# Kernel tuning notes

Measured on AMD Instinct MI355X. Metric: run time of the kernel, lower is better.

The kernel has to match this reference:

```python
import jax, jax.numpy as jnp
import numpy as np

K = 32  # neighbors per sampled point
EPS = 1e-5

def _layernorm(h, g, b):
    mu = jnp.mean(h, axis=-1, keepdims=True)
    var = jnp.mean((h - mu) ** 2, axis=-1, keepdims=True)
    return (h - mu) * jax.lax.rsqrt(var + EPS) * g + b


def setup_inputs() -> dict:
    key = jax.random.key(0)
    ks = jax.random.split(key, 20)
    N, M, D_IN, D_T = 32768, 4096, 64, 128
    s = lambda k, *sh: jax.random.normal(k, sh, dtype=jnp.float32) * 0.05
    inp = {
        "x": jax.random.normal(ks[0], (N, D_IN), dtype=jnp.float32),
        "pos": jax.random.normal(ks[1], (N, 3), dtype=jnp.float32),
        "idx": jax.random.randint(ks[2], (M,), 0, N, dtype=jnp.int32),
        "batch": jnp.zeros((N,), dtype=jnp.int32),
        # PointNetConv MLP [67 -> 128 -> 256] (ReLU after first layer only)
        "W1": s(ks[3], D_IN + 3, 128), "b1": jnp.zeros((128,), jnp.float32),
        "W2": s(ks[4], 128, 256),     "b2": jnp.zeros((256,), jnp.float32),
        # feature_reduction Linear(256, 128)
        "Wr": s(ks[5], 256, D_T), "br": jnp.zeros((D_T,), jnp.float32),
        # MultiheadAttention(128, 4)
        "in_proj_w": s(ks[6], D_T, 3 * D_T), "in_proj_b": jnp.zeros((3 * D_T,), jnp.float32),
        "out_proj_w": s(ks[7], D_T, D_T),    "out_proj_b": jnp.zeros((D_T,), jnp.float32),
        # transformer MLP [128 -> 256 -> 128]
        "Wm1": s(ks[8], D_T, 2 * D_T), "bm1": jnp.zeros((2 * D_T,), jnp.float32),
        "Wm2": s(ks[9], 2 * D_T, D_T), "bm2": jnp.zeros((D_T,), jnp.float32),
        # layer norms
        "g1": jnp.ones((D_T,), jnp.float32), "beta1": jnp.zeros((D_T,), jnp.float32),
        "g2": jnp.ones((D_T,), jnp.float32), "beta2": jnp.zeros((D_T,), jnp.float32),
    }
    return inp


def _forward(x, pos, idx, batch, W1, b1, W2, b2, Wr, br,
             in_proj_w, in_proj_b, out_proj_w, out_proj_b,
             Wm1, bm1, Wm2, bm2, g1, beta1, g2, beta2):
    q_pos = pos[idx]                                    # [M,3]
    # KNN: k nearest source points for each sampled (dst) point
    d2 = (jnp.sum(q_pos ** 2, -1, keepdims=True)
          - 2.0 * (q_pos @ pos.T)
          + jnp.sum(pos ** 2, -1)[None, :])             # [M,N]
    _, col = jax.lax.top_k(-d2, K)                      # [M,K] source indices
    # PointNetConv message: nn([x_j, pos_j - pos_i]), max-aggregate per dst
    x_j = x[col]                                        # [M,K,64]
    rel = pos[col] - q_pos[:, None, :]                  # [M,K,3]
    feat = jnp.concatenate([x_j, rel], axis=-1)         # [M,K,67]
    h = jax.nn.relu(feat @ W1 + b1) @ W2 + b2           # [M,K,256]
    agg = jnp.max(h, axis=1)                            # [M,256]
    xt = agg @ Wr + br                                  # [M,128]
    # TransformerBlock: x.view(M,1,128) -> MHA over seq len M, batch 1
    M, D = xt.shape
    H = 4
    Dh = D // H
    qkv = xt @ in_proj_w + in_proj_b                    # [M,3D]
    qh, kh, vh = [t.reshape(M, H, Dh) for t in jnp.split(qkv, 3, axis=-1)]
    scores = jnp.einsum('qhd,khd->hqk', qh, kh) / np.sqrt(Dh)
    attn = jax.nn.softmax(scores, axis=-1)
    att = jnp.einsum('hqk,khd->qhd', attn, vh).reshape(M, D)
    att = att @ out_proj_w + out_proj_b
    xt = _layernorm(xt + att, g1, beta1)
    mlp = jax.nn.relu(xt @ Wm1 + bm1) @ Wm2 + bm2
    xt = _layernorm(xt + mlp, g2, beta2)
    return xt, q_pos, batch[idx]


def reference(x, pos, idx, batch, W1, b1, W2, b2, Wr, br,
              in_proj_w, in_proj_b, out_proj_w, out_proj_b,
              Wm1, bm1, Wm2, bm2, g1, beta1, g2, beta2):
    return _forward(x, pos, idx, batch, W1, b1, W2, b2, Wr, br,
                    in_proj_w, in_proj_b, out_proj_w, out_proj_b,
                    Wm1, bm1, Wm2, bm2, g1, beta1, g2, beta2)
```

## Files before the change

### kernel.cpp

```cpp
#include <hip/hip_runtime.h>
#include <hip/hip_bf16.h>

#define DEV static __device__ __forceinline__

typedef __attribute__((ext_vector_type(8))) short          s16x8;
typedef __attribute__((ext_vector_type(8))) unsigned short u16x8;
typedef __attribute__((ext_vector_type(4))) float          f32x4;
typedef __attribute__((ext_vector_type(4))) unsigned int   u32x4;

#define MFMA16(A,B,C) __builtin_amdgcn_mfma_f32_16x16x32_bf16((A),(B),(C),0,0,0)

DEV unsigned short f2bf(float f) {
  unsigned int u = __builtin_bit_cast(unsigned int, f);
  u += 0x7fffu + ((u >> 16) & 1u);
  return (unsigned short)(u >> 16);
}
DEV float bf2f(unsigned short u) {
  unsigned int x = ((unsigned int)u) << 16;
  return __builtin_bit_cast(float, x);
}

#define QSCL 0.25503562201f

#define GRID_LO  (-5.0f)
#define GRID_IH  (3.2f)

DEV int cellc(float v) {
  int c = (int)floorf((v - GRID_LO) * GRID_IH);
  return min(31, max(0, c));
}

constexpr size_t OFF_POS4  = 0;
constexpr size_t OFF_COL   = 524288;
constexpr size_t OFF_W1T   = 1048576;
constexpr size_t OFF_W2T   = OFF_W1T  + 24576;
constexpr size_t OFF_WRT   = OFF_W2T  + 65536;
constexpr size_t OFF_WQKVT = OFF_WRT  + 65536;
constexpr size_t OFF_WOUTT = OFF_WQKVT+ 98304;
constexpr size_t OFF_WM1T  = OFF_WOUTT+ 32768;
constexpr size_t OFF_WM2T  = OFF_WM1T + 65536;
constexpr size_t OFF_H     = OFF_WM2T + 65536;
constexpr size_t OFF_SPOS    = OFF_H;
constexpr size_t OFF_CELLCNT = OFF_H + 524288;
constexpr size_t OFF_CELLDSC = OFF_H + 655360;
constexpr size_t OFF_FILL    = OFF_H + 917504;
constexpr size_t OFF_PO      = OFF_H;
constexpr size_t OFF_PL      = OFF_H + 16777216;
constexpr size_t OFF_AGG   = OFF_H    + 33554432;
constexpr size_t OFF_XT0   = OFF_AGG  + 4194304;
constexpr size_t OFF_QKV   = OFF_XT0  + 2097152;
constexpr size_t OFF_ATT   = OFF_QKV  + 6291456;
constexpr size_t OFF_PRE   = OFF_ATT  + 2097152;
constexpr size_t OFF_XT1   = OFF_PRE  + 2097152;
constexpr size_t OFF_MLP1  = OFF_XT1  + 2097152;
constexpr size_t OFF_SBIAS = OFF_MLP1 + 4194304;

__global__ __launch_bounds__(256) void zero_k(int* __restrict__ p) {
  p[blockIdx.x * 256 + threadIdx.x] = 0;
}

__global__ __launch_bounds__(256) void prep_k(
    const float* __restrict__ pos, const float* __restrict__ W1,
    const float* __restrict__ W2, const float* __restrict__ Wr,
    const float* __restrict__ ipw, const float* __restrict__ ipb,
    const float* __restrict__ opw,
    const float* __restrict__ Wm1, const float* __restrict__ Wm2,
    float4* __restrict__ pos4, unsigned short* __restrict__ w1t,
    unsigned short* __restrict__ w2t, unsigned short* __restrict__ wrt,
    unsigned short* __restrict__ wqkvt, unsigned short* __restrict__ woutt,
    unsigned short* __restrict__ wm1t, unsigned short* __restrict__ wm2t,
    int* __restrict__ cellcnt, float* __restrict__ sbias) {
  int T = blockIdx.x * 256 + threadIdx.x;
  if (T < 32768) {
    float px = pos[T*3], py = pos[T*3+1], pz = pos[T*3+2];
    pos4[T] = make_float4(px, py, pz, 0.f);
    int cid = (cellc(pz)*32 + cellc(py))*32 + cellc(px);
    atomicAdd(&cellcnt[cid], 1);
    return;
  }
  T -= 32768;
  if (T < 128*96)  { int n=T/96,  k=T%96;  w1t[T]  = f2bf(k < 67 ? W1[k*128+n] : 0.f); return; }
  T -= 128*96;
  if (T < 256*128) { int n=T/128, k=T%128; w2t[T]  = f2bf(W2[k*256+n]);  return; }
  T -= 256*128;
  if (T < 128*256) { int n=T/256, k=T%256; wrt[T]  = f2bf(Wr[k*128+n]);  return; }
  T -= 128*256;
  if (T < 384*128) { int n=T/128, k=T%128;
                     float v = ipw[k*384+n];
                     if (n < 128) v *= QSCL;
                     wqkvt[T]= f2bf(v); return; }
  T -= 384*128;
  if (T < 128*128) { int n=T/128, k=T%128; woutt[T]= f2bf(opw[k*128+n]); return; }
  T -= 128*128;
  if (T < 256*128) { int n=T/128, k=T%128; wm1t[T] = f2bf(Wm1[k*256+n]); return; }
  T -= 256*128;
  if (T < 128*256) { int n=T/256, k=T%256; wm2t[T] = f2bf(Wm2[k*128+n]); return; }
  T -= 128*256;
  if (T < 384) { sbias[T] = ipb[T] * (T < 128 ? QSCL : 1.f); return; }
}

__global__ __launch_bounds__(1024) void prefix_k(const int* __restrict__ cnt,
                                                 int2* __restrict__ desc,
                                                 int* __restrict__ fill) {
  __shared__ int wsum[16];
  const int tid = threadIdx.x, lane = tid & 63, w = tid >> 6;
  int loc[32]; int s = 0;
  #pragma unroll
  for (int i = 0; i < 32; ++i) { loc[i] = cnt[tid*32 + i]; s += loc[i]; }
  int sc = s;
  #pragma unroll
  for (int off = 1; off < 64; off <<= 1) {
    int v = __shfl_up(sc, off);
    if (lane >= off) sc += v;
  }
  if (lane == 63) wsum[w] = sc;
  __syncthreads();
  if (tid == 0) {
    int run = 0;
    #pragma unroll
    for (int i = 0; i < 16; ++i) { int v = wsum[i]; wsum[i] = run; run += v; }
  }
  __syncthreads();
  int base = wsum[w] + (sc - s);
  #pragma unroll
  for (int i = 0; i < 32; ++i) {
    int c = tid*32 + i;
    desc[c] = make_int2(base, loc[i]);
    fill[c] = base;
    base += loc[i];
  }
}

__global__ __launch_bounds__(256) void scatter_k(const float4* __restrict__ pos4,
                                                 int* __restrict__ fill,
                                                 float4* __restrict__ spos) {
  int T = blockIdx.x * 256 + threadIdx.x;
  float4 p = pos4[T];
  int cid = (cellc(p.z)*32 + cellc(p.y))*32 + cellc(p.x);
  int slot = atomicAdd(&fill[cid], 1);
  spos[slot] = make_float4(p.x, p.y, p.z, __int_as_float(T));
}

#define KNN_CAP  320
#define KNN_TRIG 192
#define KNN_KEEP 33
#define KNN_INF  3e37f

__global__ __launch_bounds__(256) void knn_k(
    const float4* __restrict__ spos, const int2* __restrict__ desc,
    const float4* __restrict__ pos4, const int* __restrict__ idx,
    int* __restrict__ col,
    float* __restrict__ outqpos, float* __restrict__ outbatch) {
  __shared__ float bufd[4][KNN_CAP];
  __shared__ int   bufi[4][KNN_CAP];
  __shared__ int   shist[4][64];
  __shared__ int2  segs[4][128];
  const int tid = threadIdx.x, lane = tid & 63, w = tid >> 6;
  const unsigned long long ltmask = (1ull << lane) - 1ull;

  const int q = blockIdx.x * 4 + w;
  const int iq = idx[q];
  const float4 qp = pos4[iq];
  const float qx = qp.x, qy = qp.y, qz = qp.z;
  const int cx0 = cellc(qx), cy0 = cellc(qy), cz0 = cellc(qz);

  float t = KNN_INF;
  int cnt = 0;

  auto compact = [&]() {
    int c_ = min(cnt, KNN_CAP);
    float vd[5]; int vi[5], bs[5]; bool okv[5];
    float dmax = 1e-30f;
    #pragma unroll
    for (int s = 0; s < 5; ++s) {
      int o2 = s*64 + lane;
      okv[s] = o2 < c_;
      vd[s] = okv[s] ? bufd[w][o2] : 0.f;
      vi[s] = okv[s] ? bufi[w][o2] : 0;
      dmax = fmaxf(dmax, vd[s]);
    }
    #pragma unroll
    for (int off = 1; off < 64; off <<= 1) dmax = fmaxf(dmax, __shfl_xor(dmax, off));
    float scale = 63.99f / dmax;
    shist[w][lane] = 0;
    #pragma unroll
    for (int s = 0; s < 5; ++s) {
      bs[s] = okv[s] ? min(63, (int)(vd[s] * scale)) : 64;
      if (okv[s]) atomicAdd(&shist[w][bs[s]], 1);
    }
    int h = shist[w][lane];
    #pragma unroll
    for (int off = 1; off < 64; off <<= 1) {
      int v = __shfl_up(h, off);
      if (lane >= off) h += v;
    }
    unsigned long long mk = __ballot(h >= KNN_KEEP);
    int E = mk ? (__ffsll((long long)mk) - 1) : 63;
    int base = 0;
    #pragma unroll
    for (int s = 0; s < 5; ++s) {
      bool keep = okv[s] && bs[s] <= E;
      unsigned long long km = __ballot(keep);
      int pp = base + (int)__popcll(km & ltmask);
      if (keep) { bufd[w][pp] = vd[s]; bufi[w][pp] = vi[s]; }
      base += (int)__popcll(km);
    }
    cnt = base;
    t = fminf(t, (float)(E + 1) / scale);
  };

  auto scan_rows = [&](int knew, int kold) {
    const int S = 2*knew + 1;
    const int NR = S*S;
    const float invS = 1.f / (float)S;
    for (int r0 = 0; r0 < NR; r0 += 64) {
      int r = r0 + lane;
      bool v = r < NR;
      int dz = (int)((float)r * invS);
      int rem = r - dz*S;
      if (rem < 0) { dz--; rem += S; } else if (rem >= S) { dz++; rem -= S; }
      int ccz = cz0 + dz - knew, ccy = cy0 + rem - knew;
      bool rowok = v && ccz >= 0 && ccz < 32 && ccy >= 0 && ccy < 32;
      bool inner = kold >= 0 && abs(dz - knew) <= kold && abs(rem - knew) <= kold;
      int cbase = (ccz*32 + ccy) * 32;
      int sL = 0, lL = 0, sR = 0, lR = 0;
      if (rowok) {
        int xa = max(cx0 - knew, 0);
        int xb = inner ? (cx0 - kold - 1) : min(cx0 + knew, 31);
        if (xa <= xb) {
          int2 d0 = desc[cbase + xa];
          int2 d1 = desc[cbase + xb];
          sL = d0.x; lL = d1.x + d1.y - d0.x;
        }
        if (inner) {
          int xa2 = cx0 + kold + 1, xb2 = min(cx0 + knew, 31);
          if (xa2 <= xb2 && xa2 >= 0) {
            int2 d0 = desc[cbase + xa2];
            int2 d1 = desc[cbase + xb2];
            sR = d0.x; lR = d1.x + d1.y - d0.x;
          }
        }
      }
      int cumL = lL;
      #pragma unroll
      for (int off = 1; off < 64; off <<= 1) {
        int vv = __shfl_up(cumL, off);
        if (lane >= off) cumL += vv;
      }
      int sumL = __shfl(cumL, 63);
      int cumR = lR;
      #pragma unroll
      for (int off = 1; off < 64; off <<= 1) {
        int vv = __shfl_up(cumR, off);
        if (lane >= off) cumR += vv;
      }
      int sumR = __shfl(cumR, 63);
      segs[w][lane]      = make_int2(sL, cumL - lL);
      segs[w][64 + lane] = make_int2(sR, sumL + cumR - lR);
      const int total = sumL + sumR;

      for (int b = 0; b < total; b += 320) {
        float d2v[5]; int piv[5]; bool hv[5];
        #pragma unroll
        for (int s5 = 0; s5 < 5; ++s5) {
          int p = b + s5*64 + lane;
          bool act = p < total;
          hv[s5] = false; d2v[s5] = 0.f; piv[s5] = 0;
          if (act) {
            int lo = 0;
            #pragma unroll
            for (int st = 64; st > 0; st >>= 1)
              if (segs[w][lo + st].y <= p) lo += st;
            int2 e = segs[w][lo];
            float4 pt = spos[e.x + (p - e.y)];
            float ddx = qx-pt.x, ddy = qy-pt.y, ddz = qz-pt.z;
            float d2 = ddx*ddx + ddy*ddy + ddz*ddz;
            d2v[s5] = d2; piv[s5] = __float_as_int(pt.w);
            hv[s5] = d2 < t;
          }
        }
        #pragma unroll
        for (int s5 = 0; s5 < 5; ++s5) {
          unsigned long long hm = __ballot(hv[s5]);
          if (hm) {
            int pp = cnt + (int)__popcll(hm & ltmask);
            if (hv[s5] && pp < KNN_CAP) { bufd[w][pp] = d2v[s5]; bufi[w][pp] = piv[s5]; }
            cnt += (int)__popcll(hm);
            if (cnt >= KNN_TRIG) compact();
          }
        }
      }
    }
  };

  auto bound32 = [&]() -> float {
    int c_ = min(cnt, KNN_CAP);
    float vv[5]; bool okv[5];
    float dmax = 1e-30f;
    #pragma unroll
    for (int s = 0; s < 5; ++s) {
      int o2 = s*64 + lane;
      okv[s] = o2 < c_;
      vv[s] = okv[s] ? bufd[w][o2] : 0.f;
      dmax = fmaxf(dmax, vv[s]);
    }
    #pragma unroll
    for (int off = 1; off < 64; off <<= 1) dmax = fmaxf(dmax, __shfl_xor(dmax, off));
    float scale = 63.99f / dmax;
    shist[w][lane] = 0;
    #pragma unroll
    for (int s = 0; s < 5; ++s)
      if (okv[s]) atomicAdd(&shist[w][min(63, (int)(vv[s] * scale))], 1);
    int h = shist[w][lane];
    #pragma unroll
    for (int off = 1; off < 64; off <<= 1) {
      int v = __shfl_up(h, off);
      if (lane >= off) h += v;
    }
    unsigned long long m = __ballot(h >= 32);
    int E = m ? (__ffsll((long long)m) - 1) : 63;
    return (float)(E + 1) / scale;
  };

  int kcur = 1;
  scan_rows(1, -1);
  for (int it = 0; it < 64; ++it) {
    if (cnt >= 32) {
      float t32u = bound32();
      t = fminf(t, t32u);
      int kneed = (int)(__builtin_sqrtf(t32u) * GRID_IH) + 1;
      if (kneed <= kcur || kcur >= 31) break;
      int knew = min(kneed, 31);
      scan_rows(knew, kcur);
      kcur = knew;
    } else {
      if (kcur >= 31) break;
      int knew = min(kcur + (cnt == 0 ? 2 : 1), 31);
      scan_rows(knew, kcur);
      kcur = knew;
    }
  }

  {
    int c_ = min(cnt, KNN_CAP);
    float vd[5]; int vi[5], bs[5]; bool okf[5];
    float dmax = 1e-30f;
    #pragma unroll
    for (int s = 0; s < 5; ++s) {
      int o2 = s*64 + lane;
      okf[s] = o2 < c_;
      vd[s] = okf[s] ? bufd[w][o2] : KNN_INF;
      vi[s] = okf[s] ? bufi[w][o2] : 0;
      dmax = fmaxf(dmax, okf[s] ? vd[s] : 0.f);
    }
    #pragma unroll
    for (int off = 1; off < 64; off <<= 1) dmax = fmaxf(dmax, __shfl_xor(dmax, off));
    float sc64 = 63.99f / dmax;
    shist[w][lane] = 0;
    #pragma unroll
    for (int s = 0; s < 5; ++s) {
      bs[s] = okf[s] ? min(63, (int)(vd[s] * sc64)) : 64;
      if (okf[s]) atomicAdd(&shist[w][bs[s]], 1);
    }
    int h = shist[w][lane];
    #pragma unroll
    for (int off = 1; off < 64; off <<= 1) {
      int v = __shfl_up(h, off);
      if (lane >= off) h += v;
    }
    unsigned long long m = __ballot(h >= 32);
    int E = m ? (__ffsll((long long)m) - 1) : 63;
    int c0 = (E > 0) ? __shfl(h, E - 1) : 0;
    int base = 0;
    #pragma unroll
    for (int s = 0; s < 5; ++s) {
      bool wr = okf[s] && (bs[s] < E);
      unsigned long long km = __ballot(wr);
      int pp = base + (int)__popcll(km & ltmask);
      if (wr) col[q*32 + pp] = vi[s];
      base += (int)__popcll(km);
    }
    #pragma unroll
    for (int s = 0; s < 5; ++s)
      if (!(okf[s] && bs[s] == E)) vd[s] = KNN_INF;
    int r = 32 - c0;
    #pragma unroll 1
    for (int kk = 0; kk < r; ++kk) {
      float bd = vd[0]; int bi = vi[0]; int bc = lane*8;
      #pragma unroll
      for (int s = 1; s < 5; ++s)
        if (vd[s] < bd) { bd = vd[s]; bi = vi[s]; bc = lane*8 + s; }
      #pragma unroll
      for (int off = 1; off < 64; off <<= 1) {
        float od = __shfl_xor(bd, off);
        int   oi = __shfl_xor(bi, off);
        int   oc = __shfl_xor(bc, off);
        if (od < bd || (od == bd && oc < bc)) { bd = od; bi = oi; bc = oc; }
      }
      if ((bc >> 3) == lane) {
        int sl = bc & 7;
        #pragma unroll
        for (int s = 0; s < 5; ++s) if (sl == s) vd[s] = KNN_INF;
      }
      if (lane == 0) col[q*32 + c0 + kk] = bi;
    }
  }
  if (lane == 0) {
    outqpos[q*3+0] = qx; outqpos[q*3+1] = qy; outqpos[q*3+2] = qz;
    outbatch[q] = 0.f;
  }
}

#define LA1(r,c) S[(r)*104 + (c)]
#define LB1(r,c) S[13312 + (r)*104 + (c)]
#define HB(r,c)  S[(r)*136 + (c)]
#define W2C(r,c) S[17408 + (r)*136 + (c)]

__global__ __launch_bounds__(256) void conv_k(
    const float* __restrict__ x, const float4* __restrict__ pos4,
    const int* __restrict__ idx, const int* __restrict__ col,
    const unsigned short* __restrict__ w1t, const float* __restrict__ b1,
    const unsigned short* __restrict__ w2t, const float* __restrict__ b2,
    float* __restrict__ agg) {
  __shared__ __align__(16) unsigned short S[26624];
  __shared__ int   sci[128];
  __shared__ float sqp[4][3];
  const int tid = threadIdx.x, lane = tid & 63, w = tid >> 6;
  const int wm = w >> 1, wn = w & 1;
  const int m0 = blockIdx.x * 4;

  if (tid < 128) sci[tid] = col[m0*32 + tid];
  if (tid >= 128 && tid < 132) {
    int m = m0 + tid - 128;
    float4 p = pos4[idx[m]];
    sqp[tid-128][0] = p.x; sqp[tid-128][1] = p.y; sqp[tid-128][2] = p.z;
  }
  #pragma unroll
  for (int rnd = 0; rnd < 6; ++rnd) {
    int e = (rnd*256 + tid) * 8;
    int n = e / 96, k = e % 96;
    *(u16x8*)&LB1(n, k) = *(const u16x8*)&w1t[e];
  }
  __syncthreads();

  {
    int r = tid >> 1, half = tid & 1;
    int ci = sci[r];
    const float* src = x + (size_t)ci*64 + half*32;
    #pragma unroll
    for (int c = 0; c < 4; ++c) {
      float4 va = ((const float4*)src)[c*2], vb = ((const float4*)src)[c*2+1];
      u16x8 v;
      v[0]=f2bf(va.x); v[1]=f2bf(va.y); v[2]=f2bf(va.z); v[3]=f2bf(va.w);
      v[4]=f2bf(vb.x); v[5]=f2bf(vb.y); v[6]=f2bf(vb.z); v[7]=f2bf(vb.w);
      *(u16x8*)&LA1(r, half*32 + c*8) = v;
    }
  }
  if (tid < 128) {
    int r = tid, g = r >> 5;
    float4 p = pos4[sci[r]];
    u16x8 z;
    #pragma unroll
    for (int e = 0; e < 8; ++e) z[e] = 0;
    u16x8 v0 = z;
    v0[0] = f2bf(p.x - sqp[g][0]); v0[1] = f2bf(p.y - sqp[g][1]); v0[2] = f2bf(p.z - sqp[g][2]);
    *(u16x8*)&LA1(r, 64) = v0;
    #pragma unroll
    for (int c = 1; c < 5; ++c) *(u16x8*)&LA1(r, 64 + c*8) = z;
  }
  __syncthreads();

  f32x4 acc[4][4];
  #pragma unroll
  for (int nf = 0; nf < 4; ++nf) {
    float bv = b1[wn*64 + nf*16 + (lane & 15)];
    #pragma unroll
    for (int mf = 0; mf < 4; ++mf) acc[mf][nf] = f32x4{bv, bv, bv, bv};
  }
  #pragma unroll
  for (int kc = 0; kc < 3; ++kc) {
    s16x8 af[4], bf_[4];
    #pragma unroll
    for (int mf = 0; mf < 4; ++mf)
      af[mf] = *(const s16x8*)&LA1(wm*64 + mf*16 + (lane&15), kc*32 + (lane>>4)*8);
    #pragma unroll
    for (int nf = 0; nf < 4; ++nf)
      bf_[nf] = *(const s16x8*)&LB1(wn*64 + nf*16 + (lane&15), kc*32 + (lane>>4)*8);
    #pragma unroll
    for (int mf = 0; mf < 4; ++mf)
      #pragma unroll
      for (int nf = 0; nf < 4; ++nf)
        acc[mf][nf] = MFMA16(af[mf], bf_[nf], acc[mf][nf]);
  }
  __syncthreads();

  #pragma unroll
  for (int mf = 0; mf < 4; ++mf)
    #pragma unroll
    for (int nf = 0; nf < 4; ++nf)
      #pragma unroll
      for (int j = 0; j < 4; ++j) {
        int rloc = wm*64 + mf*16 + ((lane>>4)<<2) + j;
        int cloc = wn*64 + nf*16 + (lane & 15);
        HB(rloc, cloc) = f2bf(fmaxf(acc[mf][nf][j], 0.f));
      }
  {
    int r2 = tid >> 2, kq = (tid & 3) * 32;
    const unsigned short* src = w2t + (size_t)r2*128 + kq;
    #pragma unroll
    for (int c = 0; c < 4; ++c)
      *(u16x8*)&W2C(r2, kq + c*8) = *(const u16x8*)&src[c*8];
  }
  __syncthreads();

  #pragma unroll 1
  for (int nc = 0; nc < 4; ++nc) {
    f32x4 acc2[2][4];
    #pragma unroll
    for (int nf = 0; nf < 4; ++nf) {
      float bv = b2[nc*64 + nf*16 + (lane & 15)];
      acc2[0][nf] = f32x4{bv, bv, bv, bv};
      acc2[1][nf] = f32x4{bv, bv, bv, bv};
    }
    #pragma unroll
    for (int ks = 0; ks < 4; ++ks) {
      s16x8 af[2], bf_[4];
      #pragma unroll
      for (int mf = 0; mf < 2; ++mf)
        af[mf] = *(const s16x8*)&HB(w*32 + mf*16 + (lane&15), ks*32 + (lane>>4)*8);
      #pragma unroll
      for (int nf = 0; nf < 4; ++nf)
        bf_[nf] = *(const s16x8*)&W2C(nf*16 + (lane&15), ks*32 + (lane>>4)*8);
      #pragma unroll
      for (int mf = 0; mf < 2; ++mf)
        #pragma unroll
        for (int nf = 0; nf < 4; ++nf)
          acc2[mf][nf] = MFMA16(af[mf], bf_[nf], acc2[mf][nf]);
    }
    #pragma unroll
    for (int nf = 0; nf < 4; ++nf) {
      float mx = acc2[0][nf][0];
      #pragma unroll
      for (int j = 1; j < 4; ++j) mx = fmaxf(mx, acc2[0][nf][j]);
      #pragma unroll
      for (int j = 0; j < 4; ++j) mx = fmaxf(mx, acc2[1][nf][j]);
      mx = fmaxf(mx, __shfl_xor(mx, 16));
      mx = fmaxf(mx, __shfl_xor(mx, 32));
      if (lane < 16) agg[(size_t)(m0 + w)*256 + nc*64 + nf*16 + lane] = mx;
    }
    if (nc < 3) {
      __syncthreads();
      int r2 = tid >> 2, kq = (tid & 3) * 32;
      const unsigned short* src = w2t + (size_t)((nc+1)*64 + r2)*128 + kq;
      #pragma unroll
      for (int c = 0; c < 4; ++c)
        *(u16x8*)&W2C(r2, kq + c*8) = *(const u16x8*)&src[c*8];
      __syncthreads();
    }
  }
}

template<int KFULL, int NFULL, bool RELU, bool HAS_RES, bool OBF16>
__global__ __launch_bounds__(256) void gemm_k(
    const float* __restrict__ A, const unsigned short* __restrict__ Bt,
    const float* __restrict__ bias, const float* __restrict__ res,
    float* __restrict__ out) {
  __shared__ unsigned short lA[64][72];
  __shared__ unsigned short lB[64][72];
  const int tid = threadIdx.x, lane = tid & 63, w = tid >> 6;
  const int m0 = blockIdx.x * 64, n0 = blockIdx.y * 64;

  f32x4 acc[4];
  #pragma unroll
  for (int nf = 0; nf < 4; ++nf) {
    float bv = bias[n0 + nf*16 + (lane & 15)];
    acc[nf] = f32x4{bv, bv, bv, bv};
  }

  for (int kb = 0; kb < KFULL; kb += 64) {
    __syncthreads();
    {
      int r = tid >> 2, kq = (tid & 3) * 16;
      const float* src = A + (size_t)(m0 + r)*KFULL + kb + kq;
      #pragma unroll
      for (int c = 0; c < 2; ++c) {
        float4 va = ((const float4*)src)[c*2], vb = ((const float4*)src)[c*2+1];
        u16x8 v;
        v[0]=f2bf(va.x); v[1]=f2bf(va.y); v[2]=f2bf(va.z); v[3]=f2bf(va.w);
        v[4]=f2bf(vb.x); v[5]=f2bf(vb.y); v[6]=f2bf(vb.z); v[7]=f2bf(vb.w);
        *(u16x8*)&lA[r][kq + c*8] = v;
      }
      const unsigned short* srcb = Bt + (size_t)(n0 + r)*KFULL + kb + kq;
      #pragma unroll
      for (int c = 0; c < 2; ++c)
        *(u16x8*)&lB[r][kq + c*8] = *(const u16x8*)&srcb[c*8];
    }
    __syncthreads();
    #pragma unroll
    for (int ks = 0; ks < 2; ++ks) {
      s16x8 af = *(const s16x8*)&lA[w*16 + (lane&15)][ks*32 + (lane>>4)*8];
      s16x8 bf_[4];
      #pragma unroll
      for (int nf = 0; nf < 4; ++nf)
        bf_[nf] = *(const s16x8*)&lB[nf*16 + (lane&15)][ks*32 + (lane>>4)*8];
      #pragma unroll
      for (int nf = 0; nf < 4; ++nf)
        acc[nf] = MFMA16(af, bf_[nf], acc[nf]);
    }
  }
  #pragma unroll
  for (int nf = 0; nf < 4; ++nf)
    #pragma unroll
    for (int j = 0; j < 4; ++j) {
      int row = m0 + w*16 + ((lane>>4)<<2) + j;
      int colg = n0 + nf*16 + (lane & 15);
      float v = acc[nf][j];
      if (HAS_RES) v += res[(size_t)row*NFULL + colg];
      if (RELU)    v = fmaxf(v, 0.f);
      if (OBF16) ((unsigned short*)out)[(size_t)row*NFULL + colg] = f2bf(v);
      else       out[(size_t)row*NFULL + colg] = v;
    }
}

template<int KFULL, bool COMBINE>
__global__ __launch_bounds__(256) void gemmln2_k(
    const float* __restrict__ A,
    const unsigned short* __restrict__ po, const float* __restrict__ pl,
    const unsigned short* __restrict__ Bt, const float* __restrict__ bias,
    const float* __restrict__ res,
    const float* __restrict__ gam, const float* __restrict__ bet,
    float* __restrict__ out) {
  constexpr int KP = KFULL + 8;
  __shared__ __align__(16) unsigned short lA[16 * KP];
  __shared__ float vout[16 * 132];
  const int tid = threadIdx.x, lane = tid & 63, w = tid >> 6;
  const int g = lane >> 4, ln_ = lane & 15;
  const int m0 = blockIdx.x * 16;

  {
    int r = tid >> 4, seg = tid & 15;
    int row = m0 + r;
    if (COMBINE) {
      int hh = seg >> 2;
      float lsum = 0.f;
      #pragma unroll
      for (int s = 0; s < 4; ++s) lsum += pl[((s*4 + hh) << 12) + row];
      float inv = 1.f / lsum;
      float a[8] = {0,0,0,0,0,0,0,0};
      #pragma unroll
      for (int s = 0; s < 4; ++s) {
        u16x8 v = *(const u16x8*)&po[((size_t)s*4096 + row)*128 + seg*8];
        #pragma unroll
        for (int e = 0; e < 8; ++e) a[e] += bf2f(v[e]);
      }
      u16x8 ov;
      #pragma unroll
      for (int e = 0; e < 8; ++e) ov[e] = f2bf(a[e] * inv);
      *(u16x8*)&lA[r*KP + seg*8] = ov;
    } else {
      const float* src = A + (size_t)row*KFULL + seg*(KFULL/16);
      #pragma unroll
      for (int c = 0; c < KFULL/128; ++c) {
        float4 va = ((const float4*)src)[c*2], vb = ((const float4*)src)[c*2+1];
        u16x8 v;
        v[0]=f2bf(va.x); v[1]=f2bf(va.y); v[2]=f2bf(va.z); v[3]=f2bf(va.w);
        v[4]=f2bf(vb.x); v[5]=f2bf(vb.y); v[6]=f2bf(vb.z); v[7]=f2bf(vb.w);
        *(u16x8*)&lA[r*KP + seg*(KFULL/16) + c*8] = v;
      }
    }
  }
  __syncthreads();

  const int n0 = w * 32;
  f32x4 acc[2];
  #pragma unroll
  for (int nf = 0; nf < 2; ++nf) {
    float bv = bias[n0 + nf*16 + ln_];
    acc[nf] = f32x4{bv, bv, bv, bv};
  }
  #pragma unroll
  for (int ks = 0; ks < KFULL/32; ++ks) {
    s16x8 af = *(const s16x8*)&lA[ln_*KP + ks*32 + g*8];
    #pragma unroll
    for (int nf = 0; nf < 2; ++nf) {
      s16x8 bf_ = *(const s16x8*)&Bt[(size_t)(n0 + nf*16 + ln_)*KFULL + ks*32 + g*8];
      acc[nf] = MFMA16(af, bf_, acc[nf]);
    }
  }
  #pragma unroll
  for (int nf = 0; nf < 2; ++nf)
    #pragma unroll
    for (int j = 0; j < 4; ++j)
      vout[(g*4 + j)*132 + n0 + nf*16 + ln_] = acc[nf][j];
  __syncthreads();

  {
    int r = tid >> 4, seg = tid & 15;
    int row = m0 + r;
    float v[8]; float sm = 0.f;
    #pragma unroll
    for (int nf = 0; nf < 8; ++nf) {
      int c = nf*16 + seg;
      float xx = vout[r*132 + c] + res[(size_t)row*128 + c];
      v[nf] = xx; sm += xx;
    }
    sm += __shfl_xor(sm, 1); sm += __shfl_xor(sm, 2);
    sm += __shfl_xor(sm, 4); sm += __shfl_xor(sm, 8);
    float mu = sm * 0.0078125f;
    float qv = 0.f;
    #pragma unroll
    for (int nf = 0; nf < 8; ++nf) { float d = v[nf] - mu; qv += d*d; }
    qv += __shfl_xor(qv, 1); qv += __shfl_xor(qv, 2);
    qv += __shfl_xor(qv, 4); qv += __shfl_xor(qv, 8);
    float rr = rsqrtf(qv * 0.0078125f + 1e-5f);
    #pragma unroll
    for (int nf = 0; nf < 8; ++nf) {
      int c = nf*16 + seg;
      out[(size_t)row*128 + c] = (v[nf] - mu) * rr * gam[c] + bet[c];
    }
  }
}

__global__ __launch_bounds__(256) void mlpln_k(
    const float* __restrict__ xt1,
    const unsigned short* __restrict__ wm1t, const float* __restrict__ bm1,
    const unsigned short* __restrict__ wm2t, const float* __restrict__ bm2,
    const float* __restrict__ gam, const float* __restrict__ bet,
    float* __restrict__ out) {
  __shared__ __align__(16) unsigned short lA[16 * 136];
  __shared__ __align__(16) unsigned short lH[16 * 264];
  __shared__ float vout[16 * 132];
  const int tid = threadIdx.x, lane = tid & 63, w = tid >> 6;
  const int g = lane >> 4, ln_ = lane & 15;
  const int m0 = blockIdx.x * 16;

  {
    int r = tid >> 4, seg = tid & 15;
    const float* src = xt1 + (size_t)(m0 + r)*128 + seg*8;
    float4 va = ((const float4*)src)[0], vb = ((const float4*)src)[1];
    u16x8 v;
    v[0]=f2bf(va.x); v[1]=f2bf(va.y); v[2]=f2bf(va.z); v[3]=f2bf(va.w);
    v[4]=f2bf(vb.x); v[5]=f2bf(vb.y); v[6]=f2bf(vb.z); v[7]=f2bf(vb.w);
    *(u16x8*)&lA[r*136 + seg*8] = v;
  }
  __syncthreads();

  {
    const int n0 = w * 64;
    f32x4 acc1[4];
    #pragma unroll
    for (int nf = 0; nf < 4; ++nf) {
      float bv = bm1[n0 + nf*16 + ln_];
      acc1[nf] = f32x4{bv, bv, bv, bv};
    }
    #pragma unroll
    for (int ks = 0; ks < 4; ++ks) {
      s16x8 af = *(const s16x8*)&lA[ln_*136 + ks*32 + g*8];
      #pragma unroll
      for (int nf = 0; nf < 4; ++nf) {
        s16x8 bf_ = *(const s16x8*)&wm1t[(size_t)(n0 + nf*16 + ln_)*128 + ks*32 + g*8];
        acc1[nf] = MFMA16(af, bf_, acc1[nf]);
      }
    }
    #pragma unroll
    for (int nf = 0; nf < 4; ++nf)
      #pragma unroll
      for (int j = 0; j < 4; ++j)
        lH[(g*4 + j)*264 + n0 + nf*16 + ln_] = f2bf(fmaxf(acc1[nf][j], 0.f));
  }
  __syncthreads();

  {
    const int n0 = w * 32;
    f32x4 acc2[2];
    #pragma unroll
    for (int nf = 0; nf < 2; ++nf) {
      float bv = bm2[n0 + nf*16 + ln_];
      acc2[nf] = f32x4{bv, bv, bv, bv};
    }
    #pragma unroll
    for (int ks = 0; ks < 8; ++ks) {
      s16x8 af = *(const s16x8*)&lH[ln_*264 + ks*32 + g*8];
      #pragma unroll
      for (int nf = 0; nf < 2; ++nf) {
        s16x8 bf_ = *(const s16x8*)&wm2t[(size_t)(n0 + nf*16 + ln_)*256 + ks*32 + g*8];
        acc2[nf] = MFMA16(af, bf_, acc2[nf]);
      }
    }
    #pragma unroll
    for (int nf = 0; nf < 2; ++nf)
      #pragma unroll
      for (int j = 0; j < 4; ++j)
        vout[(g*4 + j)*132 + n0 + nf*16 + ln_] = acc2[nf][j];
  }
  __syncthreads();

  {
    int r = tid >> 4, seg = tid & 15;
    int row = m0 + r;
    float v[8]; float sm = 0.f;
    #pragma unroll
    for (int nf = 0; nf < 8; ++nf) {
      int c = nf*16 + seg;
      float xx = vout[r*132 + c] + xt1[(size_t)row*128 + c];
      v[nf] = xx; sm += xx;
    }
    sm += __shfl_xor(sm, 1); sm += __shfl_xor(sm, 2);
    sm += __shfl_xor(sm, 4); sm += __shfl_xor(sm, 8);
    float mu = sm * 0.0078125f;
    float qv = 0.f;
    #pragma unroll
    for (int nf = 0; nf < 8; ++nf) { float d = v[nf] - mu; qv += d*d; }
    qv += __shfl_xor(qv, 1); qv += __shfl_xor(qv, 2);
    qv += __shfl_xor(qv, 4); qv += __shfl_xor(qv, 8);
    float rr = rsqrtf(qv * 0.0078125f + 1e-5f);
    #pragma unroll
    for (int nf = 0; nf < 8; ++nf) {
      int c = nf*16 + seg;
      out[(size_t)row*128 + c] = (v[nf] - mu) * rr * gam[c] + bet[c];
    }
  }
}

__global__ __launch_bounds__(256) void attn_k(
    const unsigned short* __restrict__ qkvb,
    unsigned short* __restrict__ po, float* __restrict__ pl) {
  __shared__ unsigned short lK[128][40];
  __shared__ unsigned short lV[32][136];
  const int tid = threadIdx.x, lane = tid & 63, w = tid >> 6;
  const int hh = blockIdx.y, sp = blockIdx.z;
  const int qr = blockIdx.x * 64 + w * 16;
  const int g = lane >> 4, q = lane & 15;

  s16x8 qf = *(const s16x8*)&qkvb[(size_t)(qr + q)*384 + hh*32 + g*8];

  f32x4 o[2];
  o[0] = f32x4{0.f,0.f,0.f,0.f}; o[1] = f32x4{0.f,0.f,0.f,0.f};
  float lrun = 0.f;

  const int srcA = q | ((2*(g & 1)) << 4);
  const int srcB = srcA + 16;
  const bool hi = (g >> 1) != 0;

  for (int kt = sp*8; kt < sp*8 + 8; ++kt) {
    const int k0 = kt * 128;
    __syncthreads();
    {
      int key = tid >> 1, d0 = (tid & 1) * 16;
      const unsigned short* src = qkvb + (size_t)(k0 + key)*384 + 128 + hh*32 + d0;
      *(u16x8*)&lK[key][d0]     = *(const u16x8*)&src[0];
      *(u16x8*)&lK[key][d0 + 8] = *(const u16x8*)&src[8];
    }
    {
      int kp = tid & 63, gg = tid >> 6;
      const unsigned short* s0 = qkvb + (size_t)(k0 + 2*kp)*384 + 256 + hh*32 + gg*8;
      u16x8 e0 = *(const u16x8*)s0;
      u16x8 e1 = *(const u16x8*)(s0 + 384);
      #pragma unroll
      for (int d = 0; d < 8; ++d) {
        unsigned int pkk = (unsigned int)e0[d] | ((unsigned int)e1[d] << 16);
        *(unsigned int*)&lV[gg*8 + d][2*kp] = pkk;
      }
    }
    __syncthreads();

    unsigned int pk[8][2];
    float ps = 0.f;
    #pragma unroll
    for (int nf = 0; nf < 8; ++nf) {
      s16x8 kf = *(const s16x8*)&lK[nf*16 + q][g*8];
      f32x4 c = MFMA16(kf, qf, (f32x4{0.f,0.f,0.f,0.f}));
      float p0 = exp2f(c[0]), p1 = exp2f(c[1]);
      float p2 = exp2f(c[2]), p3 = exp2f(c[3]);
      ps += (p0 + p1) + (p2 + p3);
      unsigned int u0 = __builtin_bit_cast(unsigned int, p0) + 0x8000u;
      unsigned int u1 = __builtin_bit_cast(unsigned int, p1) + 0x8000u;
      unsigned int u2 = __builtin_bit_cast(unsigned int, p2) + 0x8000u;
      unsigned int u3 = __builtin_bit_cast(unsigned int, p3) + 0x8000u;
      pk[nf][0] = (u0 >> 16) | (u1 & 0xffff0000u);
      pk[nf][1] = (u2 >> 16) | (u3 & 0xffff0000u);
    }
    ps += __shfl_xor(ps, 16);
    ps += __shfl_xor(ps, 32);
    lrun += ps;

    #pragma unroll
    for (int kc = 0; kc < 4; ++kc) {
      unsigned int a0 = (unsigned int)__shfl((int)pk[2*kc][0],   srcA);
      unsigned int b0 = (unsigned int)__shfl((int)pk[2*kc+1][0], srcA);
      unsigned int a1 = (unsigned int)__shfl((int)pk[2*kc][1],   srcA);
      unsigned int b1 = (unsigned int)__shfl((int)pk[2*kc+1][1], srcA);
      unsigned int a2 = (unsigned int)__shfl((int)pk[2*kc][0],   srcB);
      unsigned int b2 = (unsigned int)__shfl((int)pk[2*kc+1][0], srcB);
      unsigned int a3 = (unsigned int)__shfl((int)pk[2*kc][1],   srcB);
      unsigned int b3 = (unsigned int)__shfl((int)pk[2*kc+1][1], srcB);
      u32x4 wv;
      wv[0] = hi ? b0 : a0; wv[1] = hi ? b1 : a1;
      wv[2] = hi ? b2 : a2; wv[3] = hi ? b3 : a3;
      s16x8 pa = __builtin_bit_cast(s16x8, wv);
      #pragma unroll
      for (int df = 0; df < 2; ++df) {
        s16x8 vf = *(const s16x8*)&lV[df*16 + q][kc*32 + g*8];
        o[df] = MFMA16(pa, vf, o[df]);
      }
    }
  }
  #pragma unroll
  for (int df = 0; df < 2; ++df)
    #pragma unroll
    for (int j = 0; j < 4; ++j) {
      int row = qr + g*4 + j;
      po[((size_t)sp*4096 + row)*128 + hh*32 + df*16 + q] = f2bf(o[df][j]);
    }
  if (lane < 16)
    pl[((sp*4 + hh) << 12) + qr + lane] = lrun;
}

extern "C" void kernel_launch(void* const* d_in, const int* in_sizes, int n_in,
                              void* d_out, int out_size, void* d_ws, size_t ws_size,
                              hipStream_t stream) {
  const float* x    = (const float*)d_in[0];
  const float* pos  = (const float*)d_in[1];
  const int*   idx  = (const int*)d_in[2];
  const float* W1   = (const float*)d_in[4];
  const float* b1   = (const float*)d_in[5];
  const float* W2   = (const float*)d_in[6];
  const float* b2   = (const float*)d_in[7];
  const float* Wr   = (const float*)d_in[8];
  const float* br   = (const float*)d_in[9];
  const float* ipw  = (const float*)d_in[10];
  const float* ipb  = (const float*)d_in[11];
  const float* opw  = (const float*)d_in[12];
  const float* opb  = (const float*)d_in[13];
  const float* Wm1  = (const float*)d_in[14];
  const float* bm1  = (const float*)d_in[15];
  const float* Wm2  = (const float*)d_in[16];
  const float* bm2  = (const float*)d_in[17];
  const float* g1   = (const float*)d_in[18];
  const float* be1  = (const float*)d_in[19];
  const float* g2   = (const float*)d_in[20];
  const float* be2  = (const float*)d_in[21];
  float* out = (float*)d_out;
  char* ws = (char*)d_ws;

  float4*         pos4  = (float4*)(ws + OFF_POS4);
  int*            colp  = (int*)(ws + OFF_COL);
  unsigned short* w1t   = (unsigned short*)(ws + OFF_W1T);
  unsigned short* w2t   = (unsigned short*)(ws + OFF_W2T);
  unsigned short* wrt   = (unsigned short*)(ws + OFF_WRT);
  unsigned short* wqkvt = (unsigned short*)(ws + OFF_WQKVT);
  unsigned short* woutt = (unsigned short*)(ws + OFF_WOUTT);
  unsigned short* wm1t  = (unsigned short*)(ws + OFF_WM1T);
  unsigned short* wm2t  = (unsigned short*)(ws + OFF_WM2T);
  float4* sposp = (float4*)(ws + OFF_SPOS);
  int*    ccnt  = (int*)(ws + OFF_CELLCNT);
  int2*   cdesc = (int2*)(ws + OFF_CELLDSC);
  int*    cfill = (int*)(ws + OFF_FILL);
  unsigned short* pou = (unsigned short*)(ws + OFF_PO);
  float*  plp   = (float*)(ws + OFF_PL);
  float* aggp  = (float*)(ws + OFF_AGG);
  float* xt0p  = (float*)(ws + OFF_XT0);
  unsigned short* qkvb = (unsigned short*)(ws + OFF_QKV);
  float* xt1p  = (float*)(ws + OFF_XT1);
  float* sbias = (float*)(ws + OFF_SBIAS);

  zero_k<<<128, 256, 0, stream>>>(ccnt);
  prep_k<<<946, 256, 0, stream>>>(pos, W1, W2, Wr, ipw, ipb, opw, Wm1, Wm2,
                                  pos4, w1t, w2t, wrt, wqkvt, woutt, wm1t, wm2t,
                                  ccnt, sbias);
  prefix_k<<<1, 1024, 0, stream>>>(ccnt, cdesc, cfill);
  scatter_k<<<128, 256, 0, stream>>>(pos4, cfill, sposp);
  knn_k<<<1024, 256, 0, stream>>>(sposp, cdesc, pos4, idx, colp,
                                  out + 524288, out + 536576);
  conv_k<<<1024, 256, 0, stream>>>(x, pos4, idx, colp, w1t, b1, w2t, b2, aggp);
  gemm_k<256, 128, false, false, false><<<dim3(64, 2), 256, 0, stream>>>(aggp, wrt, br, nullptr, xt0p);
  gemm_k<128, 384, false, false, true><<<dim3(64, 6), 256, 0, stream>>>(xt0p, wqkvt, sbias, nullptr, (float*)qkvb);
  attn_k<<<dim3(64, 4, 4), 256, 0, stream>>>(qkvb, pou, plp);
  gemmln2_k<128, true><<<256, 256, 0, stream>>>(nullptr, pou, plp, woutt, opb, xt0p, g1, be1, xt1p);
  mlpln_k<<<256, 256, 0, stream>>>(xt1p, wm1t, bm1, wm2t, bm2, g2, be2, out);
}
```

Before: 156.6 us.

## Split attention keys into 8 partitions and compute row sums via MFMA

Doubles the key-split factor of the attention kernel (8 partitions of 512 keys instead of 4 of 1024) and updates the combine step in the output-projection kernel to sum 8 partials. Row sums of the softmax numerators are now accumulated with an extra MFMA against a ones-vector instead of VALU adds and cross-lane shuffles, and the fp32-to-bf16 packing uses the hardware packed-convert instruction. This aims to raise occupancy and cut VALU work, at the cost of twice the partial-output traffic and workspace for the combine.

```diff
diff --git a/kernel.cpp b/kernel.cpp
--- a/kernel.cpp
+++ b/kernel.cpp
@@ -644,11 +644,11 @@
       int hh = seg >> 2;
       float lsum = 0.f;
       #pragma unroll
-      for (int s = 0; s < 4; ++s) lsum += pl[((s*4 + hh) << 12) + row];
+      for (int s = 0; s < 8; ++s) lsum += pl[((s*4 + hh) << 12) + row];
       float inv = 1.f / lsum;
       float a[8] = {0,0,0,0,0,0,0,0};
       #pragma unroll
-      for (int s = 0; s < 4; ++s) {
+      for (int s = 0; s < 8; ++s) {
         u16x8 v = *(const u16x8*)&po[((size_t)s*4096 + row)*128 + seg*8];
         #pragma unroll
         for (int e = 0; e < 8; ++e) a[e] += bf2f(v[e]);
@@ -834,15 +834,22 @@
 
   s16x8 qf = *(const s16x8*)&qkvb[(size_t)(qr + q)*384 + hh*32 + g*8];
 
-  f32x4 o[2];
+  f32x4 o[2], ol;
   o[0] = f32x4{0.f,0.f,0.f,0.f}; o[1] = f32x4{0.f,0.f,0.f,0.f};
-  float lrun = 0.f;
+  ol = f32x4{0.f,0.f,0.f,0.f};
+
+  s16x8 onesf;
+  {
+    short ov = (q == 0) ? (short)0x3F80 : (short)0;
+    #pragma unroll
+    for (int e = 0; e < 8; ++e) onesf[e] = ov;
+  }
 
   const int srcA = q | ((2*(g & 1)) << 4);
   const int srcB = srcA + 16;
   const bool hi = (g >> 1) != 0;
 
-  for (int kt = sp*8; kt < sp*8 + 8; ++kt) {
+  for (int kt = sp*4; kt < sp*4 + 4; ++kt) {
     const int k0 = kt * 128;
     __syncthreads();
     {
@@ -865,24 +872,18 @@
     __syncthreads();
 
     unsigned int pk[8][2];
-    float ps = 0.f;
     #pragma unroll
     for (int nf = 0; nf < 8; ++nf) {
       s16x8 kf = *(const s16x8*)&lK[nf*16 + q][g*8];
       f32x4 c = MFMA16(kf, qf, (f32x4{0.f,0.f,0.f,0.f}));
       float p0 = exp2f(c[0]), p1 = exp2f(c[1]);
       float p2 = exp2f(c[2]), p3 = exp2f(c[3]);
-      ps += (p0 + p1) + (p2 + p3);
-      unsigned int u0 = __builtin_bit_cast(unsigned int, p0) + 0x8000u;
-      unsigned int u1 = __builtin_bit_cast(unsigned int, p1) + 0x8000u;
-      unsigned int u2 = __builtin_bit_cast(unsigned int, p2) + 0x8000u;
-      unsigned int u3 = __builtin_bit_cast(unsigned int, p3) + 0x8000u;
-      pk[nf][0] = (u0 >> 16) | (u1 & 0xffff0000u);
-      pk[nf][1] = (u2 >> 16) | (u3 & 0xffff0000u);
-    }
-    ps += __shfl_xor(ps, 16);
-    ps += __shfl_xor(ps, 32);
-    lrun += ps;
+      unsigned int r0, r1;
+      asm("v_cvt_pk_bf16_f32 %0, %1, %2" : "=v"(r0) : "v"(p0), "v"(p1));
+      asm("v_cvt_pk_bf16_f32 %0, %1, %2" : "=v"(r1) : "v"(p2), "v"(p3));
+      pk[nf][0] = r0;
+      pk[nf][1] = r1;
+    }
 
     #pragma unroll
     for (int kc = 0; kc < 4; ++kc) {
@@ -903,6 +904,7 @@
         s16x8 vf = *(const s16x8*)&lV[df*16 + q][kc*32 + g*8];
         o[df] = MFMA16(pa, vf, o[df]);
       }
+      ol = MFMA16(pa, onesf, ol);
     }
   }
   #pragma unroll
@@ -912,8 +914,11 @@
       int row = qr + g*4 + j;
       po[((size_t)sp*4096 + row)*128 + hh*32 + df*16 + q] = f2bf(o[df][j]);
     }
-  if (lane < 16)
-    pl[((sp*4 + hh) << 12) + qr + lane] = lrun;
+  if (q == 0) {
+    #pragma unroll
+    for (int j = 0; j < 4; ++j)
+      pl[((sp*4 + hh) << 12) + qr + g*4 + j] = ol[j];
+  }
 }
 
 extern "C" void kernel_launch(void* const* d_in, const int* in_sizes, int n_in,
@@ -975,7 +980,7 @@
   conv_k<<<1024, 256, 0, stream>>>(x, pos4, idx, colp, w1t, b1, w2t, b2, aggp);
   gemm_k<256, 128, false, false, false><<<dim3(64, 2), 256, 0, stream>>>(aggp, wrt, br, nullptr, xt0p);
   gemm_k<128, 384, false, false, true><<<dim3(64, 6), 256, 0, stream>>>(xt0p, wqkvt, sbias, nullptr, (float*)qkvb);
-  attn_k<<<dim3(64, 4, 4), 256, 0, stream>>>(qkvb, pou, plp);
+  attn_k<<<dim3(64, 4, 8), 256, 0, stream>>>(qkvb, pou, plp);
   gemmln2_k<128, true><<<256, 256, 0, stream>>>(nullptr, pou, plp, woutt, opb, xt0p, g1, be1, xt1p);
   mlpln_k<<<256, 256, 0, stream>>>(xt1p, wm1t, bm1, wm2t, bm2, g2, be2, out);
 }
```

Result: faster. 153.4 us (-2.1%).
